# Performance work log

Measured on AMD Instinct MI355X. Metric: run time of the kernel, lower is better.

Reference implementation:

```python
import jax, jax.numpy as jnp
import numpy as np

N_NODES = 50000
N_EDGES = 800000
D_IN = 788
D_HID = 256
N_REL = 7
N_CLS = 2


def rgcn_conv(x, w_rel, w_root, b, src, dst, edge_type):
    """PyG RGCNConv with default mean aggregation per relation + root weight + bias.
    x: (N, F_in); w_rel: (R, F_in, F_out); w_root: (F_in, F_out); b: (F_out,).
    src/dst: (E,) with edge_index[0]=source j, edge_index[1]=target i.
    """
    R, _, F_out = w_rel.shape
    N = x.shape[0]
    # transform-then-gather (equivalent to PyG's gather-then-transform, cheaper)
    x_rel = jnp.einsum('nf,rfo->rno', x, w_rel)          # (R, N, F_out)
    msg = x_rel[edge_type, src]                           # (E, F_out)
    agg = jnp.zeros((R, N, F_out), x.dtype).at[edge_type, dst].add(msg)
    cnt = jnp.zeros((R, N), x.dtype).at[edge_type, dst].add(1.0)
    out = (agg / jnp.clip(cnt, 1.0)[..., None]).sum(0)    # mean per relation, summed over relations
    return out + x @ w_root + b


def setup_inputs() -> dict:
    key = jax.random.key(0)
    ks = jax.random.split(key, 9)
    x = jax.random.normal(ks[0], (N_NODES, D_IN), dtype=jnp.float32)
    edge_index = jax.random.randint(ks[1], (2, N_EDGES), 0, N_NODES, dtype=jnp.int64)
    edge_type = jax.random.randint(ks[2], (N_EDGES,), 0, N_REL, dtype=jnp.int64)
    s1 = 0.05
    w1_rel = jax.random.normal(ks[3], (N_REL, D_IN, D_HID), dtype=jnp.float32) * s1
    w1_root = jax.random.normal(ks[4], (D_IN, D_HID), dtype=jnp.float32) * s1
    b1 = jnp.zeros((D_HID,), dtype=jnp.float32)
    w2_rel = jax.random.normal(ks[5], (N_REL, D_HID, N_CLS), dtype=jnp.float32) * s1
    w2_root = jax.random.normal(ks[6], (D_HID, N_CLS), dtype=jnp.float32) * s1
    b2 = jnp.zeros((N_CLS,), dtype=jnp.float32)
    return {"x": x, "edge_index": edge_index, "edge_type": edge_type,
            "w1_rel": w1_rel, "w1_root": w1_root, "b1": b1,
            "w2_rel": w2_rel, "w2_root": w2_root, "b2": b2}


def reference(x, edge_index, edge_type, w1_rel, w1_root, b1, w2_rel, w2_root, b2):
    src, dst = edge_index[0], edge_index[1]
    h = jax.nn.relu(rgcn_conv(x, w1_rel, w1_root, b1, src, dst, edge_type))
    # F.dropout(p=0.5) is identity in eval mode
    out = rgcn_conv(h, w2_rel, w2_root, b2, src, dst, edge_type)
    return out
```

## Files before the change

### kernel.cpp

```cpp
#include <hip/hip_runtime.h>
#include <hip/hip_bf16.h>
#include <stdint.h>

#define N_NODES 50000
#define N_EDGES 800000
#define D_IN    788
#define D_INP   832
#define D_HID   256
#define N_REL   7
#define NBINS   (N_REL * N_NODES)
#define NSCANB  342
#define NXTILE  391

typedef __attribute__((ext_vector_type(8))) short bf16x8;
typedef __attribute__((ext_vector_type(4))) float f32x4;
typedef __attribute__((ext_vector_type(4))) unsigned int u32x4;

__device__ __forceinline__ unsigned short f2bf(float f) {
  union { __hip_bfloat16 h; unsigned short u; } v;
  v.h = __float2bfloat16(f);
  return v.u;
}

__device__ __forceinline__ f32x4 bf4(ushort4 g) {
  union { unsigned int u; float f; } a, b, c, d;
  a.u = (unsigned)g.x << 16; b.u = (unsigned)g.y << 16;
  c.u = (unsigned)g.z << 16; d.u = (unsigned)g.w << 16;
  return (f32x4){a.f, b.f, c.f, d.f};
}

#define GLOAD16(g, l) __builtin_amdgcn_global_load_lds(                      \
    (const __attribute__((address_space(1))) unsigned int*)(g),              \
    (__attribute__((address_space(3))) unsigned int*)(l), 16, 0, 0)


__global__ void k_conv_w(const float* __restrict__ w_rel, const float* __restrict__ w_root,
                         unsigned short* __restrict__ wt) {
  int b = blockIdx.x;
  int m = b / 26, pc = b % 26;
  int o = threadIdx.x;
  const float* src = (m < N_REL) ? (w_rel + (size_t)m * D_IN * D_HID) : w_root;
  int cc = pc ^ (o & 1);
  int k0 = cc * 32;

  unsigned short v[32];
#pragma unroll
  for (int kk = 0; kk < 32; kk++) {
    int k = k0 + kk;
    v[kk] = (k < D_IN) ? f2bf(src[(size_t)k * D_HID + o]) : (unsigned short)0;
  }

  unsigned short* dst = wt + ((size_t)m * D_HID + o) * D_INP + pc * 32;
  int sw = (o >> 1) & 3;
#pragma unroll
  for (int g = 0; g < 4; g++) {
    union { unsigned short us[8]; u32x4 u; } pk;
#pragma unroll
    for (int j = 0; j < 8; j++) pk.us[j] = v[g * 8 + j];
    *(u32x4*)(dst + (g ^ sw) * 8) = pk.u;
  }
}

__global__ void k_xbf(const float* __restrict__ x, unsigned short* __restrict__ xb) {
  int t = blockIdx.x * blockDim.x + threadIdx.x;
  if (t >= N_NODES * 104) return;
  int n = t / 104, gi = t % 104;
  int pc = gi >> 2, p = gi & 3;
  int cc = pc ^ (n & 1);
  int g = p ^ ((n >> 1) & 3);
  int c = cc * 32 + g * 8;
  union { unsigned short us[8]; u32x4 v; } pk;
  if (c + 7 < D_IN) {
    float4 a = *(const float4*)(x + (size_t)n * D_IN + c);
    float4 b = *(const float4*)(x + (size_t)n * D_IN + c + 4);
    pk.us[0] = f2bf(a.x); pk.us[1] = f2bf(a.y); pk.us[2] = f2bf(a.z); pk.us[3] = f2bf(a.w);
    pk.us[4] = f2bf(b.x); pk.us[5] = f2bf(b.y); pk.us[6] = f2bf(b.z); pk.us[7] = f2bf(b.w);
  } else {
#pragma unroll
    for (int j = 0; j < 8; j++)
      pk.us[j] = (c + j < D_IN) ? f2bf(x[(size_t)n * D_IN + c + j]) : (unsigned short)0;
  }
  *(u32x4*)(xb + (size_t)n * D_INP + pc * 32 + p * 8) = pk.v;
}

__global__ void k_count(const int* __restrict__ etype, const int* __restrict__ edst,
                        int* __restrict__ cnt) {
  int t = blockIdx.x * blockDim.x + threadIdx.x;
  if (t >= N_EDGES) return;
  atomicAdd(&cnt[etype[t] * N_NODES + edst[t]], 1);
}

__global__ void k_scan1(const int* __restrict__ cnt, int* __restrict__ bsum) {
  __shared__ int wsh[4];
  int b = blockIdx.x, tid = threadIdx.x;
  int base = b * 1024 + tid * 4;
  int4 v = {0, 0, 0, 0};
  if (base + 3 < NBINS) v = *(const int4*)(cnt + base);
  else { for (int i = 0; i < 4; i++) if (base + i < NBINS) ((int*)&v)[i] = cnt[base + i]; }
  int s = v.x + v.y + v.z + v.w;
  for (int o = 32; o > 0; o >>= 1) s += __shfl_down(s, o);
  if ((tid & 63) == 0) wsh[tid >> 6] = s;
  __syncthreads();
  if (tid == 0) bsum[b] = wsh[0] + wsh[1] + wsh[2] + wsh[3];
}

__global__ void k_scan2(const int* __restrict__ bsum, int* __restrict__ boff) {
  __shared__ int tmp[512];
  int tid = threadIdx.x;
  int mine = (tid < NSCANB) ? bsum[tid] : 0;
  tmp[tid] = mine;
  __syncthreads();
  for (int o = 1; o < 512; o <<= 1) {
    int v = (tid >= o) ? tmp[tid - o] : 0;
    __syncthreads();
    tmp[tid] += v;
    __syncthreads();
  }
  if (tid < NSCANB) boff[tid] = tmp[tid] - mine;
}

__global__ void k_scan3(const int* __restrict__ cnt, const int* __restrict__ boff,
                        int* __restrict__ S) {
  __shared__ int wsum[4];
  int b = blockIdx.x, tid = threadIdx.x;
  int base = b * 1024 + tid * 4;
  int4 v = {0, 0, 0, 0};
  if (base + 3 < NBINS) v = *(const int4*)(cnt + base);
  else { for (int i = 0; i < 4; i++) if (base + i < NBINS) ((int*)&v)[i] = cnt[base + i]; }
  int s = v.x + v.y + v.z + v.w;
  int lane = tid & 63, w = tid >> 6;
  int sc = s;
  for (int o = 1; o < 64; o <<= 1) { int u = __shfl_up(sc, o); if (lane >= o) sc += u; }
  if (lane == 63) wsum[w] = sc;
  __syncthreads();
  int wbase = 0;
  for (int i = 0; i < w; i++) wbase += wsum[i];
  int excl = boff[b] + wbase + sc - s;
  int o0 = excl, o1 = excl + v.x, o2 = o1 + v.y, o3 = o2 + v.z;
  if (base + 3 < NBINS) { int4 o4 = {o0, o1, o2, o3}; *(int4*)(S + base) = o4; }
  else {
    if (base     < NBINS) S[base]     = o0;
    if (base + 1 < NBINS) S[base + 1] = o1;
    if (base + 2 < NBINS) S[base + 2] = o2;
    if (base + 3 < NBINS) S[base + 3] = o3;
  }
}

__global__ void k_scatter(const int* __restrict__ etype, const int* __restrict__ edst,
                          const int* __restrict__ esrc, const int* __restrict__ S,
                          int* __restrict__ rank, int* __restrict__ psrc) {
  int t = blockIdx.x * blockDim.x + threadIdx.x;
  if (t >= N_EDGES) return;
  int bin = etype[t] * N_NODES + edst[t];
  int r = atomicAdd(&rank[bin], 1);
  psrc[S[bin] + r] = esrc[t];
}

template<int SWZ, int NMAT>
__global__ __launch_bounds__(512) void k_gemm_g(
    const unsigned short* __restrict__ xb, const unsigned short* __restrict__ wt,
    unsigned short* __restrict__ xrs, int mb) {
  __shared__ __align__(16) unsigned short As[128 * 64];
  __shared__ __align__(16) unsigned short Bs[256 * 64];

  int tid = threadIdx.x;
  int bx, by;
  if (SWZ) {
    int b = blockIdx.x;
    int l = (b % 8) * (NXTILE * NMAT / 8) + b / 8;
    bx = l / NMAT; by = l % NMAT;
  } else {
    bx = blockIdx.x; by = blockIdx.y;
  }
  int mat = mb + by;
  int m0 = bx * 128;
  const unsigned short* wsec = wt + (size_t)mat * (D_HID * D_INP);
  int lane = tid & 63, w = tid >> 6;
  int wm = w >> 2, wn = w & 3;

  int sr = tid >> 3, sg = (tid & 7) * 8;
  int ar0 = m0 + sr;      if (ar0 > N_NODES - 1) ar0 = N_NODES - 1;
  int ar1 = m0 + 64 + sr; if (ar1 > N_NODES - 1) ar1 = N_NODES - 1;
  const unsigned short* asrc0 = xb + (size_t)ar0 * D_INP + sg;
  const unsigned short* asrc1 = xb + (size_t)ar1 * D_INP + sg;
  const unsigned short* bsrc0 = wsec + (size_t)sr * D_INP + sg;
  const unsigned short* bsrc1 = bsrc0 + (size_t)64 * D_INP;
  const unsigned short* bsrc2 = bsrc0 + (size_t)128 * D_INP;
  const unsigned short* bsrc3 = bsrc0 + (size_t)192 * D_INP;
  unsigned short* al0 = As + tid * 8;
  unsigned short* al1 = As + 4096 + tid * 8;
  unsigned short* bl0 = Bs + tid * 8;
  unsigned short* bl1 = Bs + 4096 + tid * 8;
  unsigned short* bl2 = Bs + 8192 + tid * 8;
  unsigned short* bl3 = Bs + 12288 + tid * 8;

  f32x4 acc[4][4];
#pragma unroll
  for (int i = 0; i < 4; i++)
#pragma unroll
    for (int j = 0; j < 4; j++) acc[i][j] = (f32x4){0.f, 0.f, 0.f, 0.f};

  int row = lane & 15, quad = lane >> 4;
  int rg = (quad ^ ((row >> 1) & 3)) * 8;
  int cp0 = (row & 1) * 32;
  int cp1 = 32 - cp0;

  for (int ks = 0; ks < 13; ks++) {
    int ko = ks * 64;
    GLOAD16(asrc0 + ko, al0);
    GLOAD16(asrc1 + ko, al1);
    GLOAD16(bsrc0 + ko, bl0);
    GLOAD16(bsrc1 + ko, bl1);
    GLOAD16(bsrc2 + ko, bl2);
    GLOAD16(bsrc3 + ko, bl3);
    __syncthreads();

    bf16x8 af[4], bfr[4];
#pragma unroll
    for (int i = 0; i < 4; i++)
      af[i] = *(const bf16x8*)(As + (wm * 64 + i * 16 + row) * 64 + cp0 + rg);
#pragma unroll
    for (int j = 0; j < 4; j++)
      bfr[j] = *(const bf16x8*)(Bs + (wn * 64 + j * 16 + row) * 64 + cp0 + rg);
#pragma unroll
    for (int i = 0; i < 4; i++)
#pragma unroll
      for (int j = 0; j < 4; j++)
        acc[i][j] = __builtin_amdgcn_mfma_f32_16x16x32_bf16(af[i], bfr[j], acc[i][j], 0, 0, 0);
#pragma unroll
    for (int i = 0; i < 4; i++)
      af[i] = *(const bf16x8*)(As + (wm * 64 + i * 16 + row) * 64 + cp1 + rg);
#pragma unroll
    for (int j = 0; j < 4; j++)
      bfr[j] = *(const bf16x8*)(Bs + (wn * 64 + j * 16 + row) * 64 + cp1 + rg);
#pragma unroll
    for (int i = 0; i < 4; i++)
#pragma unroll
      for (int j = 0; j < 4; j++)
        acc[i][j] = __builtin_amdgcn_mfma_f32_16x16x32_bf16(af[i], bfr[j], acc[i][j], 0, 0, 0);
    __syncthreads();
  }

  int col_l = lane & 15, rquad = lane >> 4;
  unsigned short* xo = xrs + (size_t)by * ((size_t)N_NODES * D_HID);
#pragma unroll
  for (int i = 0; i < 4; i++) {
#pragma unroll
    for (int reg = 0; reg < 4; reg++) {
      int node = m0 + wm * 64 + i * 16 + rquad * 4 + reg;
      if (node < N_NODES) {
#pragma unroll
        for (int j = 0; j < 4; j++)
          xo[(size_t)node * D_HID + wn * 64 + j * 16 + col_l] = f2bf(acc[i][j][reg]);
      }
    }
  }
}

__global__ __launch_bounds__(256) void k_gemm_f(
    const float* __restrict__ x, const unsigned short* __restrict__ wt,
    unsigned short* __restrict__ xrs, int mb) {
  __shared__ __align__(16) unsigned short As[64 * 40];
  __shared__ __align__(16) unsigned short Bs[256 * 40];

  int tid = threadIdx.x;
  int mat = mb + blockIdx.y;
  int m0 = blockIdx.x * 64;
  const unsigned short* wsec = wt + (size_t)mat * (D_HID * D_INP);
  int lane = tid & 63, w = tid >> 6;

  int ra = tid >> 2, ca = tid & 3, ca8 = ca * 8;
  int ra1 = ra & 1;
  int arow = m0 + ra; if (arow > N_NODES - 1) arow = N_NODES - 1;
  const float* apf = x + (size_t)arow * D_IN;
  const unsigned short* bgp = wsec + (size_t)ra * D_INP + (ca ^ ((ra >> 1) & 3)) * 8;
  unsigned short* al = As + ra * 40 + ca8;
  unsigned short* bl = Bs + ra * 40 + ca8;

  f32x4 acc[4][4];
#pragma unroll
  for (int i = 0; i < 4; i++)
#pragma unroll
    for (int j = 0; j < 4; j++) acc[i][j] = (f32x4){0.f, 0.f, 0.f, 0.f};

  float4 pa0 = *(const float4*)(apf + ca8);
  float4 pa1 = *(const float4*)(apf + ca8 + 4);
  int kb0 = ra1 * 32;
  u32x4 pb0 = *(const u32x4*)(bgp + kb0);
  u32x4 pb1 = *(const u32x4*)(bgp + kb0 +  64 * D_INP);
  u32x4 pb2 = *(const u32x4*)(bgp + kb0 + 128 * D_INP);
  u32x4 pb3 = *(const u32x4*)(bgp + kb0 + 192 * D_INP);

  int row = lane & 15, quad = lane >> 4;
  for (int ks = 0; ks < 25; ks++) {
    if (ks < 24) {
      union { unsigned short us[8]; u32x4 v; } pk;
      pk.us[0] = f2bf(pa0.x); pk.us[1] = f2bf(pa0.y);
      pk.us[2] = f2bf(pa0.z); pk.us[3] = f2bf(pa0.w);
      pk.us[4] = f2bf(pa1.x); pk.us[5] = f2bf(pa1.y);
      pk.us[6] = f2bf(pa1.z); pk.us[7] = f2bf(pa1.w);
      *(u32x4*)al = pk.v;
    } else {
      float v0 = pa0.x, v1 = pa0.y, v2 = pa0.z, v3 = pa0.w;
      float v4 = pa1.x, v5 = pa1.y, v6 = pa1.z, v7 = pa1.w;
      if (ca8 == 16) { v0 = pa1.x; v1 = pa1.y; v2 = pa1.z; v3 = pa1.w;
                       v4 = 0.f; v5 = 0.f; v6 = 0.f; v7 = 0.f; }
      if (ca8 == 24) { v0 = 0.f; v1 = 0.f; v2 = 0.f; v3 = 0.f;
                       v4 = 0.f; v5 = 0.f; v6 = 0.f; v7 = 0.f; }
      union { unsigned short us[8]; u32x4 v; } pk;
      pk.us[0] = f2bf(v0); pk.us[1] = f2bf(v1); pk.us[2] = f2bf(v2); pk.us[3] = f2bf(v3);
      pk.us[4] = f2bf(v4); pk.us[5] = f2bf(v5); pk.us[6] = f2bf(v6); pk.us[7] = f2bf(v7);
      *(u32x4*)al = pk.v;
    }
    *(u32x4*)bl = pb0;
    *(u32x4*)(bl +  64 * 40) = pb1;
    *(u32x4*)(bl + 128 * 40) = pb2;
    *(u32x4*)(bl + 192 * 40) = pb3;
    __syncthreads();

    if (ks < 24) {
      int on = (ks + 1) * 32 + ca8;
      int lo = (on > 780) ? 780 : on;
      pa0 = *(const float4*)(apf + lo);
      pa1 = *(const float4*)(apf + lo + 4);
      int ko = ((ks + 1) ^ ra1) * 32;
      pb0 = *(const u32x4*)(bgp + ko);
      pb1 = *(const u32x4*)(bgp + ko +  64 * D_INP);
      pb2 = *(const u32x4*)(bgp + ko + 128 * D_INP);
      pb3 = *(const u32x4*)(bgp + ko + 192 * D_INP);
    }

    bf16x8 af[4], bfr[4];
#pragma unroll
    for (int i = 0; i < 4; i++)
      af[i] = *(const bf16x8*)(As + (i * 16 + row) * 40 + quad * 8);
#pragma unroll
    for (int j = 0; j < 4; j++)
      bfr[j] = *(const bf16x8*)(Bs + (w * 64 + j * 16 + row) * 40 + quad * 8);
#pragma unroll
    for (int i = 0; i < 4; i++)
#pragma unroll
      for (int j = 0; j < 4; j++)
        acc[i][j] = __builtin_amdgcn_mfma_f32_16x16x32_bf16(af[i], bfr[j], acc[i][j], 0, 0, 0);
    __syncthreads();
  }

  int col_l = lane & 15, rquad = lane >> 4;
  unsigned short* xo = xrs + (size_t)blockIdx.y * ((size_t)N_NODES * D_HID);
#pragma unroll
  for (int i = 0; i < 4; i++) {
#pragma unroll
    for (int reg = 0; reg < 4; reg++) {
      int node = m0 + i * 16 + rquad * 4 + reg;
      if (node < N_NODES) {
#pragma unroll
        for (int j = 0; j < 4; j++)
          xo[(size_t)node * D_HID + w * 64 + j * 16 + col_l] = f2bf(acc[i][j][reg]);
      }
    }
  }
}

__global__ __launch_bounds__(256) void k_agg8(
    const unsigned short* __restrict__ xrs, const int* __restrict__ S,
    const int* __restrict__ cnt, const int* __restrict__ psrc,
    const float* __restrict__ b1, const float* __restrict__ w2rel,
    const float* __restrict__ w2root, float* __restrict__ y) {
  __shared__ float hsh[4][256];
  int wv = threadIdx.x >> 6;
  int n = blockIdx.x * 4 + wv;
  int lane = threadIdx.x & 63;
  if (n >= N_NODES) return;

  int c_l = 0, p_l = 0;
  if (lane < N_REL) {
    c_l = cnt[lane * N_NODES + n];
    p_l = S[lane * N_NODES + n];
  }

  f32x4 acc = (f32x4){0.f, 0.f, 0.f, 0.f};
#pragma unroll
  for (int r = 0; r < N_REL; r++) {
    int c = __shfl(c_l, r);
    if (c > 0) {
      int p = __shfl(p_l, r);
      const unsigned short* slab = xrs + (size_t)r * N_NODES * D_HID;
      f32x4 s = (f32x4){0.f, 0.f, 0.f, 0.f};
      int e = 0;
      for (; e + 1 < c; e += 2) {
        int s0 = psrc[p + e], s1 = psrc[p + e + 1];
        ushort4 g0 = *(const ushort4*)(slab + (size_t)s0 * D_HID + lane * 4);
        ushort4 g1 = *(const ushort4*)(slab + (size_t)s1 * D_HID + lane * 4);
        s += bf4(g0) + bf4(g1);
      }
      if (e < c) {
        int s0 = psrc[p + e];
        ushort4 g0 = *(const ushort4*)(slab + (size_t)s0 * D_HID + lane * 4);
        s += bf4(g0);
      }
      acc += s * (1.0f / (float)c);
    }
  }

  ushort4 gr = *(const ushort4*)(xrs + ((size_t)7 * N_NODES + n) * D_HID + lane * 4);
  acc += bf4(gr);
  f32x4 b = *(const f32x4*)(b1 + lane * 4);
  f32x4 hv;
  hv[0] = fmaxf(acc[0] + b[0], 0.f);
  hv[1] = fmaxf(acc[1] + b[1], 0.f);
  hv[2] = fmaxf(acc[2] + b[2], 0.f);
  hv[3] = fmaxf(acc[3] + b[3], 0.f);

  *(f32x4*)&hsh[wv][lane * 4] = hv;
  __builtin_amdgcn_wave_barrier();

  int m = lane >> 3, sl = lane & 7;
  const float* wp = (m < N_REL) ? (w2rel + m * (D_HID * 2)) : w2root;
  float d0 = 0.f, d1 = 0.f;
#pragma unroll
  for (int j = 0; j < 8; j++) {
    int db = sl * 4 + j * 32;
    f32x4 h4 = *(const f32x4*)&hsh[wv][db];
    f32x4 wa = *(const f32x4*)(wp + db * 2);
    f32x4 wb = *(const f32x4*)(wp + db * 2 + 4);
    d0 += h4[0] * wa[0] + h4[1] * wa[2] + h4[2] * wb[0] + h4[3] * wb[2];
    d1 += h4[0] * wa[1] + h4[1] * wa[3] + h4[2] * wb[1] + h4[3] * wb[3];
  }
  d0 += __shfl_down(d0, 1); d1 += __shfl_down(d1, 1);
  d0 += __shfl_down(d0, 2); d1 += __shfl_down(d1, 2);
  d0 += __shfl_down(d0, 4); d1 += __shfl_down(d1, 4);
  if (sl == 0) {
    y[(size_t)m * (N_NODES * 2) + n * 2]     = d0;
    y[(size_t)m * (N_NODES * 2) + n * 2 + 1] = d1;
  }
}

__global__ __launch_bounds__(256) void k_agg(
    const unsigned short* __restrict__ xrs, const int* __restrict__ S,
    const int* __restrict__ cnt, const int* __restrict__ psrc,
    float* __restrict__ h, const float* __restrict__ b1,
    const float* __restrict__ w2rel, const float* __restrict__ w2root,
    float* __restrict__ y, int r0, int pass) {
  int n = blockIdx.x * 4 + (threadIdx.x >> 6);
  int lane = threadIdx.x & 63;
  if (n >= N_NODES) return;
  f32x4 acc;
  if (pass == 0) acc = (f32x4){0.f, 0.f, 0.f, 0.f};
  else acc = *(const f32x4*)(h + (size_t)n * D_HID + lane * 4);

  int nr = (pass < 3) ? 2 : 1;
  for (int rr = 0; rr < nr; rr++) {
    int bin = (r0 + rr) * N_NODES + n;
    int c = cnt[bin];
    if (c > 0) {
      int p = S[bin];
      f32x4 s = (f32x4){0.f, 0.f, 0.f, 0.f};
      int e = 0;
      for (; e + 1 < c; e += 2) {
        int s0 = psrc[p + e], s1 = psrc[p + e + 1];
        ushort4 g0 = *(const ushort4*)(xrs + ((size_t)rr * N_NODES + s0) * D_HID + lane * 4);
        ushort4 g1 = *(const ushort4*)(xrs + ((size_t)rr * N_NODES + s1) * D_HID + lane * 4);
        s += bf4(g0) + bf4(g1);
      }
      if (e < c) {
        int s0 = psrc[p + e];
        ushort4 g0 = *(const ushort4*)(xrs + ((size_t)rr * N_NODES + s0) * D_HID + lane * 4);
        s += bf4(g0);
      }
      acc += s * (1.0f / (float)c);
    }
  }

  if (pass < 3) {
    *(f32x4*)(h + (size_t)n * D_HID + lane * 4) = acc;
    return;
  }

  ushort4 gr = *(const ushort4*)(xrs + ((size_t)1 * N_NODES + n) * D_HID + lane * 4);
  acc += bf4(gr);
  f32x4 b = *(const f32x4*)(b1 + lane * 4);
  f32x4 hv;
  hv[0] = fmaxf(acc[0] + b[0], 0.f);
  hv[1] = fmaxf(acc[1] + b[1], 0.f);
  hv[2] = fmaxf(acc[2] + b[2], 0.f);
  hv[3] = fmaxf(acc[3] + b[3], 0.f);

#pragma unroll
  for (int m = 0; m < 8; m++) {
    const float* wp = (m < N_REL) ? (w2rel + m * (D_HID * 2)) : w2root;
    f32x4 wa = *(const f32x4*)(wp + lane * 8);
    f32x4 wb = *(const f32x4*)(wp + lane * 8 + 4);
    float d0 = hv[0] * wa[0] + hv[1] * wa[2] + hv[2] * wb[0] + hv[3] * wb[2];
    float d1 = hv[0] * wa[1] + hv[1] * wa[3] + hv[2] * wb[1] + hv[3] * wb[3];
#pragma unroll
    for (int off = 32; off > 0; off >>= 1) {
      d0 += __shfl_down(d0, off);
      d1 += __shfl_down(d1, off);
    }
    if (lane == 0) {
      y[(size_t)m * (N_NODES * 2) + n * 2]     = d0;
      y[(size_t)m * (N_NODES * 2) + n * 2 + 1] = d1;
    }
  }
}

__global__ void k_out(const float* __restrict__ y, const float* __restrict__ b2,
                      const int* __restrict__ cnt, const int* __restrict__ S,
                      const int* __restrict__ psrc, float* __restrict__ out) {
  int t = blockIdx.x * blockDim.x + threadIdx.x;
  if (t < NBINS) {
    int c = cnt[t];
    if (c == 0) return;
    int p = S[t];
    int r = t / N_NODES;
    int i = t - r * N_NODES;
    const float* yr = y + (size_t)r * (N_NODES * 2);
    float s0 = 0.f, s1 = 0.f;
    for (int e = 0; e < c; e++) {
      int sc = psrc[p + e];
      float2 v = *(const float2*)(yr + sc * 2);
      s0 += v.x; s1 += v.y;
    }
    float is = 1.0f / (float)c;
    atomicAdd(out + (size_t)i * 2,     s0 * is);
    atomicAdd(out + (size_t)i * 2 + 1, s1 * is);
  } else if (t < NBINS + N_NODES) {
    int i = t - NBINS;
    float2 v = *(const float2*)(y + (size_t)N_REL * (N_NODES * 2) + i * 2);
    atomicAdd(out + (size_t)i * 2,     v.x + b2[0]);
    atomicAdd(out + (size_t)i * 2 + 1, v.y + b2[1]);
  }
}

#define OFF_WT   0u
#define OFF_XRS  3407872u
#define OFF_H    54607872u
#define OFF_CNT  105807872u
#define OFF_RANK 107207872u
#define OFF_S    108607872u
#define OFF_PSRC 110007872u
#define OFF_Y    113207872u
#define OFF_BSUM 116407872u
#define OFF_BOFF 116409920u
#define OFF_XB   116411968u
#define WS_NEED_XB 199611968ull

#define F_OFF_WT   0u
#define F_OFF_XRS  3407872u
#define F_OFF_CNT  208207872u
#define F_OFF_RANK 209607872u
#define F_OFF_S    211007872u
#define F_OFF_PSRC 212407872u
#define F_OFF_Y    215607872u
#define F_OFF_BSUM 218807872u
#define F_OFF_BOFF 218809920u
#define F_OFF_XB   218811968u
#define WS_NEED_FULL 302011968ull

extern "C" void kernel_launch(void* const* d_in, const int* in_sizes, int n_in,
                              void* d_out, int out_size, void* d_ws, size_t ws_size,
                              hipStream_t stream) {
  const float* x      = (const float*)d_in[0];
  const int*   eidx   = (const int*)d_in[1];
  const int*   etype  = (const int*)d_in[2];
  const float* w1rel  = (const float*)d_in[3];
  const float* w1root = (const float*)d_in[4];
  const float* b1     = (const float*)d_in[5];
  const float* w2rel  = (const float*)d_in[6];
  const float* w2root = (const float*)d_in[7];
  const float* b2     = (const float*)d_in[8];
  float* out = (float*)d_out;
  char* ws = (char*)d_ws;
  const int* esrc = eidx;
  const int* edst = eidx + N_EDGES;

  const bool full = (ws_size >= WS_NEED_FULL);
  const bool big  = !full && (ws_size >= WS_NEED_XB);

  hipMemsetAsync(d_out, 0, (size_t)out_size * sizeof(float), stream);

  if (full) {
    unsigned short* wt  = (unsigned short*)(ws + F_OFF_WT);
    unsigned short* xrs = (unsigned short*)(ws + F_OFF_XRS);
    int*   cnt  = (int*)(ws + F_OFF_CNT);
    int*   rank = (int*)(ws + F_OFF_RANK);
    int*   S    = (int*)(ws + F_OFF_S);
    int*   psrc = (int*)(ws + F_OFF_PSRC);
    float* y    = (float*)(ws + F_OFF_Y);
    int*   bsum = (int*)(ws + F_OFF_BSUM);
    int*   boff = (int*)(ws + F_OFF_BOFF);
    unsigned short* xb = (unsigned short*)(ws + F_OFF_XB);

    hipMemsetAsync(ws + F_OFF_CNT, 0, 2800000u, stream);

    k_conv_w<<<8 * 26, 256, 0, stream>>>(w1rel, w1root, wt);
    k_xbf<<<(N_NODES * 104 + 255) / 256, 256, 0, stream>>>(x, xb);
    k_count<<<(N_EDGES + 255) / 256, 256, 0, stream>>>(etype, edst, cnt);
    k_scan1<<<NSCANB, 256, 0, stream>>>(cnt, bsum);
    k_scan2<<<1, 512, 0, stream>>>(bsum, boff);
    k_scan3<<<NSCANB, 256, 0, stream>>>(cnt, boff, S);
    k_scatter<<<(N_EDGES + 255) / 256, 256, 0, stream>>>(etype, edst, esrc, S, rank, psrc);

    k_gemm_g<1, 8><<<NXTILE * 8, 512, 0, stream>>>(xb, wt, xrs, 0);
    k_agg8<<<(N_NODES + 3) / 4, 256, 0, stream>>>(xrs, S, cnt, psrc,
                                                  b1, w2rel, w2root, y);
    k_out<<<(NBINS + N_NODES + 255) / 256, 256, 0, stream>>>(y, b2, cnt, S, psrc, out);
    return;
  }

  unsigned short* wt  = (unsigned short*)(ws + OFF_WT);
  unsigned short* xrs = (unsigned short*)(ws + OFF_XRS);
  float* h    = (float*)(ws + OFF_H);
  int*   cnt  = (int*)(ws + OFF_CNT);
  int*   rank = (int*)(ws + OFF_RANK);
  int*   S    = (int*)(ws + OFF_S);
  int*   psrc = (int*)(ws + OFF_PSRC);
  float* y    = (float*)(ws + OFF_Y);
  int*   bsum = (int*)(ws + OFF_BSUM);
  int*   boff = (int*)(ws + OFF_BOFF);
  unsigned short* xb = (unsigned short*)(ws + OFF_XB);

  hipMemsetAsync(ws + OFF_CNT, 0, 2800000u, stream);

  k_conv_w<<<8 * 26, 256, 0, stream>>>(w1rel, w1root, wt);
  if (big)
    k_xbf<<<(N_NODES * 104 + 255) / 256, 256, 0, stream>>>(x, xb);
  k_count<<<(N_EDGES + 255) / 256, 256, 0, stream>>>(etype, edst, cnt);
  k_scan1<<<NSCANB, 256, 0, stream>>>(cnt, bsum);
  k_scan2<<<1, 512, 0, stream>>>(bsum, boff);
  k_scan3<<<NSCANB, 256, 0, stream>>>(cnt, boff, S);
  k_scatter<<<(N_EDGES + 255) / 256, 256, 0, stream>>>(etype, edst, esrc, S, rank, psrc);

  for (int p = 0; p < 4; p++) {
    if (big)
      k_gemm_g<0, 2><<<dim3(NXTILE, 2), 512, 0, stream>>>(xb, wt, xrs, 2 * p);
    else
      k_gemm_f<<<dim3(782, 2), 256, 0, stream>>>(x, wt, xrs, 2 * p);
    k_agg<<<(N_NODES + 3) / 4, 256, 0, stream>>>(xrs, S, cnt, psrc, h,
                                                 b1, w2rel, w2root, y, 2 * p, p);
  }

  k_out<<<(NBINS + N_NODES + 255) / 256, 256, 0, stream>>>(y, b2, cnt, S, psrc, out);
}
```

Measured before the change: 682.8 us.

## Store bf16 X and weights in K-chunk-major layout for contiguous GEMM tile loads

Changes the bf16 copies of x and the weights from row-major padded rows (832 wide) to chunk-major blocks of 32 K-columns. Each GEMM K-step tile then becomes one contiguous region in global memory, which is meant to improve coalescing and DRAM locality for the global_load_lds fills. The LDS tiles are split into two 32-wide halves with matching swizzle, and the fallback GEMM's weight indexing is updated to match. The k_xbf writes now go chunk-major while its reads of x stay strided per row, which may cost more on the conversion pass.

```diff
diff --git a/kernel.cpp b/kernel.cpp
--- a/kernel.cpp
+++ b/kernel.cpp
@@ -5,7 +5,9 @@
 #define N_NODES 50000
 #define N_EDGES 800000
 #define D_IN    788
-#define D_INP   832
+#define NCHUNK  26
+#define CS_X    (N_NODES * 32)
+#define CS_W    (256 * 32)
 #define D_HID   256
 #define N_REL   7
 #define NBINS   (N_REL * N_NODES)
@@ -37,11 +39,10 @@
 __global__ void k_conv_w(const float* __restrict__ w_rel, const float* __restrict__ w_root,
                          unsigned short* __restrict__ wt) {
   int b = blockIdx.x;
-  int m = b / 26, pc = b % 26;
+  int m = b / NCHUNK, chunk = b % NCHUNK;
   int o = threadIdx.x;
   const float* src = (m < N_REL) ? (w_rel + (size_t)m * D_IN * D_HID) : w_root;
-  int cc = pc ^ (o & 1);
-  int k0 = cc * 32;
+  int k0 = chunk * 32;
 
   unsigned short v[32];
 #pragma unroll
@@ -50,7 +51,7 @@
     v[kk] = (k < D_IN) ? f2bf(src[(size_t)k * D_HID + o]) : (unsigned short)0;
   }
 
-  unsigned short* dst = wt + ((size_t)m * D_HID + o) * D_INP + pc * 32;
+  unsigned short* dst = wt + (size_t)m * (NCHUNK * CS_W) + (size_t)chunk * CS_W + o * 32;
   int sw = (o >> 1) & 3;
 #pragma unroll
   for (int g = 0; g < 4; g++) {
@@ -63,12 +64,12 @@
 
 __global__ void k_xbf(const float* __restrict__ x, unsigned short* __restrict__ xb) {
   int t = blockIdx.x * blockDim.x + threadIdx.x;
-  if (t >= N_NODES * 104) return;
-  int n = t / 104, gi = t % 104;
-  int pc = gi >> 2, p = gi & 3;
-  int cc = pc ^ (n & 1);
+  if (t >= NCHUNK * N_NODES * 4) return;
+  int chunk = t / (N_NODES * 4);
+  int rem = t - chunk * (N_NODES * 4);
+  int n = rem >> 2, p = rem & 3;
   int g = p ^ ((n >> 1) & 3);
-  int c = cc * 32 + g * 8;
+  int c = chunk * 32 + g * 8;
   union { unsigned short us[8]; u32x4 v; } pk;
   if (c + 7 < D_IN) {
     float4 a = *(const float4*)(x + (size_t)n * D_IN + c);
@@ -80,7 +81,7 @@
     for (int j = 0; j < 8; j++)
       pk.us[j] = (c + j < D_IN) ? f2bf(x[(size_t)n * D_IN + c + j]) : (unsigned short)0;
   }
-  *(u32x4*)(xb + (size_t)n * D_INP + pc * 32 + p * 8) = pk.v;
+  *(u32x4*)(xb + (size_t)chunk * CS_X + (size_t)n * 32 + p * 8) = pk.v;
 }
 
 __global__ void k_count(const int* __restrict__ etype, const int* __restrict__ edst,
@@ -160,8 +161,8 @@
 __global__ __launch_bounds__(512) void k_gemm_g(
     const unsigned short* __restrict__ xb, const unsigned short* __restrict__ wt,
     unsigned short* __restrict__ xrs, int mb) {
-  __shared__ __align__(16) unsigned short As[128 * 64];
-  __shared__ __align__(16) unsigned short Bs[256 * 64];
+  __shared__ __align__(16) unsigned short As[2 * 128 * 32];
+  __shared__ __align__(16) unsigned short Bs[2 * 256 * 32];
 
   int tid = threadIdx.x;
   int bx, by;
@@ -174,19 +175,14 @@
   }
   int mat = mb + by;
   int m0 = bx * 128;
-  const unsigned short* wsec = wt + (size_t)mat * (D_HID * D_INP);
+  const unsigned short* wsec = wt + (size_t)mat * (NCHUNK * CS_W);
   int lane = tid & 63, w = tid >> 6;
   int wm = w >> 2, wn = w & 3;
 
-  int sr = tid >> 3, sg = (tid & 7) * 8;
-  int ar0 = m0 + sr;      if (ar0 > N_NODES - 1) ar0 = N_NODES - 1;
-  int ar1 = m0 + 64 + sr; if (ar1 > N_NODES - 1) ar1 = N_NODES - 1;
-  const unsigned short* asrc0 = xb + (size_t)ar0 * D_INP + sg;
-  const unsigned short* asrc1 = xb + (size_t)ar1 * D_INP + sg;
-  const unsigned short* bsrc0 = wsec + (size_t)sr * D_INP + sg;
-  const unsigned short* bsrc1 = bsrc0 + (size_t)64 * D_INP;
-  const unsigned short* bsrc2 = bsrc0 + (size_t)128 * D_INP;
-  const unsigned short* bsrc3 = bsrc0 + (size_t)192 * D_INP;
+  int sr = tid >> 2, sg = (tid & 3) * 8;
+  int arow = m0 + sr; if (arow > N_NODES - 1) arow = N_NODES - 1;
+  const unsigned short* axb = xb + (size_t)arow * 32 + sg;
+  const unsigned short* bw  = wsec + (size_t)sr * 32 + sg;
   unsigned short* al0 = As + tid * 8;
   unsigned short* al1 = As + 4096 + tid * 8;
   unsigned short* bl0 = Bs + tid * 8;
@@ -202,42 +198,35 @@
 
   int row = lane & 15, quad = lane >> 4;
   int rg = (quad ^ ((row >> 1) & 3)) * 8;
-  int cp0 = (row & 1) * 32;
-  int cp1 = 32 - cp0;
 
   for (int ks = 0; ks < 13; ks++) {
-    int ko = ks * 64;
-    GLOAD16(asrc0 + ko, al0);
-    GLOAD16(asrc1 + ko, al1);
-    GLOAD16(bsrc0 + ko, bl0);
-    GLOAD16(bsrc1 + ko, bl1);
-    GLOAD16(bsrc2 + ko, bl2);
-    GLOAD16(bsrc3 + ko, bl3);
+    size_t cx = (size_t)(2 * ks) * CS_X;
+    int    cw = 2 * ks * CS_W;
+    GLOAD16(axb + cx, al0);
+    GLOAD16(axb + cx + CS_X, al1);
+    GLOAD16(bw + cw, bl0);
+    GLOAD16(bw + cw + 4096, bl1);
+    GLOAD16(bw + cw + CS_W, bl2);
+    GLOAD16(bw + cw + CS_W + 4096, bl3);
     __syncthreads();
 
-    bf16x8 af[4], bfr[4];
-#pragma unroll
-    for (int i = 0; i < 4; i++)
-      af[i] = *(const bf16x8*)(As + (wm * 64 + i * 16 + row) * 64 + cp0 + rg);
-#pragma unroll
-    for (int j = 0; j < 4; j++)
-      bfr[j] = *(const bf16x8*)(Bs + (wn * 64 + j * 16 + row) * 64 + cp0 + rg);
-#pragma unroll
-    for (int i = 0; i < 4; i++)
+#pragma unroll
+    for (int kk = 0; kk < 2; kk++) {
+      const unsigned short* Ac = As + kk * 4096;
+      const unsigned short* Bc = Bs + kk * 8192;
+      bf16x8 af[4], bfr[4];
+#pragma unroll
+      for (int i = 0; i < 4; i++)
+        af[i] = *(const bf16x8*)(Ac + (wm * 64 + i * 16 + row) * 32 + rg);
 #pragma unroll
       for (int j = 0; j < 4; j++)
-        acc[i][j] = __builtin_amdgcn_mfma_f32_16x16x32_bf16(af[i], bfr[j], acc[i][j], 0, 0, 0);
-#pragma unroll
-    for (int i = 0; i < 4; i++)
-      af[i] = *(const bf16x8*)(As + (wm * 64 + i * 16 + row) * 64 + cp1 + rg);
-#pragma unroll
-    for (int j = 0; j < 4; j++)
-      bfr[j] = *(const bf16x8*)(Bs + (wn * 64 + j * 16 + row) * 64 + cp1 + rg);
-#pragma unroll
-    for (int i = 0; i < 4; i++)
-#pragma unroll
-      for (int j = 0; j < 4; j++)
-        acc[i][j] = __builtin_amdgcn_mfma_f32_16x16x32_bf16(af[i], bfr[j], acc[i][j], 0, 0, 0);
+        bfr[j] = *(const bf16x8*)(Bc + (wn * 64 + j * 16 + row) * 32 + rg);
+#pragma unroll
+      for (int i = 0; i < 4; i++)
+#pragma unroll
+        for (int j = 0; j < 4; j++)
+          acc[i][j] = __builtin_amdgcn_mfma_f32_16x16x32_bf16(af[i], bfr[j], acc[i][j], 0, 0, 0);
+    }
     __syncthreads();
   }
 
@@ -266,14 +255,13 @@
   int tid = threadIdx.x;
   int mat = mb + blockIdx.y;
   int m0 = blockIdx.x * 64;
-  const unsigned short* wsec = wt + (size_t)mat * (D_HID * D_INP);
+  const unsigned short* wsec = wt + (size_t)mat * (NCHUNK * CS_W);
   int lane = tid & 63, w = tid >> 6;
 
   int ra = tid >> 2, ca = tid & 3, ca8 = ca * 8;
-  int ra1 = ra & 1;
   int arow = m0 + ra; if (arow > N_NODES - 1) arow = N_NODES - 1;
   const float* apf = x + (size_t)arow * D_IN;
-  const unsigned short* bgp = wsec + (size_t)ra * D_INP + (ca ^ ((ra >> 1) & 3)) * 8;
+  const unsigned short* bgp = wsec + (size_t)ra * 32 + (ca ^ ((ra >> 1) & 3)) * 8;
   unsigned short* al = As + ra * 40 + ca8;
   unsigned short* bl = Bs + ra * 40 + ca8;
 
@@ -285,11 +273,10 @@
 
   float4 pa0 = *(const float4*)(apf + ca8);
   float4 pa1 = *(const float4*)(apf + ca8 + 4);
-  int kb0 = ra1 * 32;
-  u32x4 pb0 = *(const u32x4*)(bgp + kb0);
-  u32x4 pb1 = *(const u32x4*)(bgp + kb0 +  64 * D_INP);
-  u32x4 pb2 = *(const u32x4*)(bgp + kb0 + 128 * D_INP);
-  u32x4 pb3 = *(const u32x4*)(bgp + kb0 + 192 * D_INP);
+  u32x4 pb0 = *(const u32x4*)(bgp);
+  u32x4 pb1 = *(const u32x4*)(bgp +  64 * 32);
+  u32x4 pb2 = *(const u32x4*)(bgp + 128 * 32);
+  u32x4 pb3 = *(const u32x4*)(bgp + 192 * 32);
 
   int row = lane & 15, quad = lane >> 4;
   for (int ks = 0; ks < 25; ks++) {
@@ -323,11 +310,11 @@
       int lo = (on > 780) ? 780 : on;
       pa0 = *(const float4*)(apf + lo);
       pa1 = *(const float4*)(apf + lo + 4);
-      int ko = ((ks + 1) ^ ra1) * 32;
+      int ko = (ks + 1) * CS_W;
       pb0 = *(const u32x4*)(bgp + ko);
-      pb1 = *(const u32x4*)(bgp + ko +  64 * D_INP);
-      pb2 = *(const u32x4*)(bgp + ko + 128 * D_INP);
-      pb3 = *(const u32x4*)(bgp + ko + 192 * D_INP);
+      pb1 = *(const u32x4*)(bgp + ko +  64 * 32);
+      pb2 = *(const u32x4*)(bgp + ko + 128 * 32);
+      pb3 = *(const u32x4*)(bgp + ko + 192 * 32);
     }
 
     bf16x8 af[4], bfr[4];
@@ -593,8 +580,8 @@
 
     hipMemsetAsync(ws + F_OFF_CNT, 0, 2800000u, stream);
 
-    k_conv_w<<<8 * 26, 256, 0, stream>>>(w1rel, w1root, wt);
-    k_xbf<<<(N_NODES * 104 + 255) / 256, 256, 0, stream>>>(x, xb);
+    k_conv_w<<<8 * NCHUNK, 256, 0, stream>>>(w1rel, w1root, wt);
+    k_xbf<<<(NCHUNK * N_NODES * 4 + 255) / 256, 256, 0, stream>>>(x, xb);
     k_count<<<(N_EDGES + 255) / 256, 256, 0, stream>>>(etype, edst, cnt);
     k_scan1<<<NSCANB, 256, 0, stream>>>(cnt, bsum);
     k_scan2<<<1, 512, 0, stream>>>(bsum, boff);
@@ -622,9 +609,9 @@
 
   hipMemsetAsync(ws + OFF_CNT, 0, 2800000u, stream);
 
-  k_conv_w<<<8 * 26, 256, 0, stream>>>(w1rel, w1root, wt);
+  k_conv_w<<<8 * NCHUNK, 256, 0, stream>>>(w1rel, w1root, wt);
   if (big)
-    k_xbf<<<(N_NODES * 104 + 255) / 256, 256, 0, stream>>>(x, xb);
+    k_xbf<<<(NCHUNK * N_NODES * 4 + 255) / 256, 256, 0, stream>>>(x, xb);
   k_count<<<(N_EDGES + 255) / 256, 256, 0, stream>>>(etype, edst, cnt);
   k_scan1<<<NSCANB, 256, 0, stream>>>(cnt, bsum);
   k_scan2<<<1, 512, 0, stream>>>(bsum, boff);
```

Result: faster. 666.4 us (-2.4%).
